# Kernel optimization log

Hardware: AMD Instinct MI355X
Metric: run time of the kernel (lower is better)

Reference implementation:

```python
import jax, jax.numpy as jnp
import numpy as np

EMBED_DIM = 1024
NUM_HEADS = 16
HEAD_DIM = EMBED_DIM // NUM_HEADS
FF_DIM = 4096
SPARSITY_FACTOR = 0.1
SPARSITY_THRESHOLD = 0.5
EPS = 1e-5


def layer_norm(x, w, b):
    mu = jnp.mean(x, axis=-1, keepdims=True)
    var = jnp.mean(jnp.square(x - mu), axis=-1, keepdims=True)
    return (x - mu) * jax.lax.rsqrt(var + EPS) * w + b


def setup_inputs() -> dict:
    key = jax.random.key(0)
    ks = jax.random.split(key, 12)
    B, N, C = 8, 1024, EMBED_DIM
    s = 0.02
    return {
        "x": jax.random.normal(ks[0], (B, N, C), jnp.float32),
        "ln1_w": jnp.ones((C,), jnp.float32),
        "ln1_b": jnp.zeros((C,), jnp.float32),
        "qkv_w": jax.random.normal(ks[1], (3 * C, C), jnp.float32) * s,
        "qkv_b": jnp.zeros((3 * C,), jnp.float32),
        "out_w": jax.random.normal(ks[2], (C, C), jnp.float32) * s,
        "out_b": jnp.zeros((C,), jnp.float32),
        "ln2_w": jnp.ones((C,), jnp.float32),
        "ln2_b": jnp.zeros((C,), jnp.float32),
        "w1": jax.random.normal(ks[3], (FF_DIM, C), jnp.float32) * s,
        "b1": jnp.zeros((FF_DIM,), jnp.float32),
        "w2": jax.random.normal(ks[4], (C, FF_DIM), jnp.float32) * s,
        "b2": jnp.zeros((C,), jnp.float32),
        "mask1": jax.random.uniform(ks[5], (B, N, FF_DIM), jnp.float32),
        "mask2": jax.random.uniform(ks[6], (B, N, C), jnp.float32),
        "layer_idx": 0,
    }


def sparse_attention(x, qkv_w, qkv_b, out_w, out_b):
    B, N, C = x.shape
    qkv = (x @ qkv_w.T + qkv_b).reshape(B, N, 3, NUM_HEADS, HEAD_DIM)
    qkv = jnp.transpose(qkv, (2, 0, 3, 1, 4))  # (3,B,H,N,hd)
    q, k, v = qkv[0], qkv[1], qkv[2]
    scale = HEAD_DIM ** (-0.5)
    scores = jnp.einsum("bhnd,bhmd->bhnm", q, k) * scale  # (B,H,N,N)
    k_sparse = int(SPARSITY_FACTOR * N)
    if 0 < k_sparse < N:
        _, idx = jax.lax.top_k(scores, k_sparse)  # (B,H,N,k)
        bi = jnp.arange(B)[:, None, None, None]
        hi = jnp.arange(NUM_HEADS)[None, :, None, None]
        ni = jnp.arange(N)[None, None, :, None]
        mask = jnp.zeros_like(scores).at[bi, hi, ni, idx].set(1.0)
        scores = scores * mask - 1e9 * (1.0 - mask)
    attn = jax.nn.softmax(scores, axis=-1)
    out = jnp.einsum("bhnm,bhmd->bhnd", attn, v)  # (B,H,N,hd)
    out = jnp.transpose(out, (0, 2, 1, 3)).reshape(B, N, C)
    return out @ out_w.T + out_b


def reference(x, ln1_w, ln1_b, qkv_w, qkv_b, out_w, out_b, ln2_w, ln2_b,
              w1, b1, w2, b2, mask1, mask2, layer_idx):
    # Attention block with residual
    x = x + sparse_attention(layer_norm(x, ln1_w, ln1_b), qkv_w, qkv_b, out_w, out_b)
    # Random-masked FFN block with residual
    m1 = (mask1 > SPARSITY_THRESHOLD).astype(x.dtype)
    m2 = (mask2 > SPARSITY_THRESHOLD).astype(x.dtype)
    h = layer_norm(x, ln2_w, ln2_b)
    h = jax.nn.relu((h @ w1.T + b1) * m1)
    h = ((h @ w2.T + b2) * m2)
    x = x + h
    # Symbolic branch: only runs when (layer_idx+1)%4==0 and never modifies x
    # (original ends in `pass`), so it is an identity on the output.
    return x
```

## Files before the change

kernel.cpp:

```cpp
#include <hip/hip_runtime.h>
#include <cstdint>
#include <cstddef>

typedef unsigned short u16;
typedef __bf16 bf16x8 __attribute__((ext_vector_type(8)));
typedef float f32x4 __attribute__((ext_vector_type(4)));

#define GLOBAL_AS __attribute__((address_space(1)))
#define LDS_AS    __attribute__((address_space(3)))

__device__ __forceinline__ float bf2f(u16 v) {
  return __builtin_bit_cast(float, (uint32_t)v << 16);
}
__device__ __forceinline__ u16 f2bf(float f) {
  uint32_t u = __builtin_bit_cast(uint32_t, f);
  u += 0x7FFFu + ((u >> 16) & 1u);
  return (u16)(u >> 16);
}
__device__ __forceinline__ float extload(const void* p, size_t i, int isf) {
  return isf ? ((const float*)p)[i] : bf2f(((const u16*)p)[i]);
}
__device__ __forceinline__ void gl_lds16(const void* g, void* l) {
  __builtin_amdgcn_global_load_lds((const GLOBAL_AS void*)g, (LDS_AS void*)l, 16, 0, 0);
}

__global__ __launch_bounds__(256) void sniff_k(const u16* __restrict__ x, int* __restrict__ flag) {
  const int t = threadIdx.x;
  int cnt = 0;
#pragma unroll
  for (int j = 0; j < 16; ++j) {
    const u16 w = x[t * 16 + j];
    const int e = (w >> 7) & 0xFF;
    cnt += (e >= 0x90) ? 1 : 0;
  }
#pragma unroll
  for (int o = 32; o; o >>= 1) cnt += __shfl_xor(cnt, o);
  __shared__ int red[4];
  if ((t & 63) == 0) red[t >> 6] = cnt;
  __syncthreads();
  if (t == 0) flag[0] = (red[0] + red[1] + red[2] + red[3] > 16) ? 1 : 0;
}

__global__ __launch_bounds__(256) void cvt_k(const void* __restrict__ in, u16* __restrict__ out,
                                             const int* __restrict__ flagp, int n) {
  const int i = (blockIdx.x * 256 + threadIdx.x) * 4;
  if (i >= n) return;
  if (*flagp) {
    const float4 v = *(const float4*)((const float*)in + i);
    out[i] = f2bf(v.x); out[i + 1] = f2bf(v.y); out[i + 2] = f2bf(v.z); out[i + 3] = f2bf(v.w);
  } else {
    *(ushort4*)(out + i) = *(const ushort4*)((const u16*)in + i);
  }
}

template<bool INTF32>
__global__ __launch_bounds__(256) void ln_k(const void* __restrict__ inp,
                                            const void* __restrict__ w,
                                            const void* __restrict__ b,
                                            u16* __restrict__ out,
                                            const int* __restrict__ flagp)
{
  const int isf = *flagp;
  const int row = blockIdx.x;
  const int t = threadIdx.x;
  float x0, x1, x2, x3;
  if (INTF32 || isf) {
    const float4 vv = ((const float4*)((const float*)inp + (size_t)row * 1024))[t];
    x0 = vv.x; x1 = vv.y; x2 = vv.z; x3 = vv.w;
  } else {
    const ushort4 vv = ((const ushort4*)((const u16*)inp + (size_t)row * 1024))[t];
    x0 = bf2f(vv.x); x1 = bf2f(vv.y); x2 = bf2f(vv.z); x3 = bf2f(vv.w);
  }
  float s = x0 + x1 + x2 + x3;
  float sq = x0 * x0 + x1 * x1 + x2 * x2 + x3 * x3;
#pragma unroll
  for (int o = 32; o; o >>= 1) { s += __shfl_xor(s, o); sq += __shfl_xor(sq, o); }
  __shared__ float red[8];
  const int wv = t >> 6;
  if ((t & 63) == 0) { red[wv] = s; red[wv + 4] = sq; }
  __syncthreads();
  s = red[0] + red[1] + red[2] + red[3];
  sq = red[4] + red[5] + red[6] + red[7];
  const float mu = s * (1.0f / 1024.0f);
  const float var = sq * (1.0f / 1024.0f) - mu * mu;
  const float rstd = rsqrtf(var + 1e-5f);
  const int c0 = t * 4;
  u16* o4 = out + (size_t)row * 1024 + c0;
  o4[0] = f2bf((x0 - mu) * rstd * extload(w, c0 + 0, isf) + extload(b, c0 + 0, isf));
  o4[1] = f2bf((x1 - mu) * rstd * extload(w, c0 + 1, isf) + extload(b, c0 + 1, isf));
  o4[2] = f2bf((x2 - mu) * rstd * extload(w, c0 + 2, isf) + extload(b, c0 + 2, isf));
  o4[3] = f2bf((x3 - mu) * rstd * extload(w, c0 + 3, isf) + extload(b, c0 + 3, isf));
}

template<int EPI>
__global__ __launch_bounds__(256, 2) void gemm_bt(
    const u16* __restrict__ A, const u16* __restrict__ B,
    const void* __restrict__ bias, const void* __restrict__ auxb,
    const float* __restrict__ auxf, void* __restrict__ outp,
    int M, int N, int K, const int* __restrict__ flagp)
{
  __shared__ u16 sA[128 * 32];
  __shared__ u16 sB[128 * 32];
  const int t = threadIdx.x;
  const int lane = t & 63;
  const int wv = t >> 6;
  const int wm = (wv >> 1) << 6;
  const int wn = (wv & 1) << 6;
  const int bm = blockIdx.y << 7;
  const int bn = blockIdx.x << 7;

  f32x4 acc[4][4] = {};

  const int ldr = t >> 2;
  const int lseg = t & 3;
  const int fr = lane & 15;
  const int q = lane >> 4;

  for (int kt = 0; kt < K; kt += 32) {
    __syncthreads();
#pragma unroll
    for (int i = 0; i < 2; ++i) {
      const int r = ldr + (i << 6);
      const int sl = lseg ^ ((r >> 1) & 3);
      gl_lds16(A + (size_t)(bm + r) * K + kt + (sl << 3), &sA[(((i << 8) + t) << 3)]);
      gl_lds16(B + (size_t)(bn + r) * K + kt + (sl << 3), &sB[(((i << 8) + t) << 3)]);
    }
    asm volatile("s_waitcnt vmcnt(0)" ::: "memory");
    __syncthreads();

    bf16x8 af[4], bfv[4];
#pragma unroll
    for (int i = 0; i < 4; ++i) {
      const int rr = wm + (i << 4) + fr;
      af[i] = *(const bf16x8*)&sA[(rr << 5) + ((q ^ ((rr >> 1) & 3)) << 3)];
      const int nn = wn + (i << 4) + fr;
      bfv[i] = *(const bf16x8*)&sB[(nn << 5) + ((q ^ ((nn >> 1) & 3)) << 3)];
    }
#pragma unroll
    for (int mi = 0; mi < 4; ++mi)
#pragma unroll
      for (int ni = 0; ni < 4; ++ni)
        acc[mi][ni] = __builtin_amdgcn_mfma_f32_16x16x32_bf16(af[mi], bfv[ni], acc[mi][ni], 0, 0, 0);
  }

  const int isf = *flagp;
#pragma unroll
  for (int mi = 0; mi < 4; ++mi) {
#pragma unroll
    for (int ni = 0; ni < 4; ++ni) {
#pragma unroll
      for (int r = 0; r < 4; ++r) {
        const int gm = bm + wm + (mi << 4) + (q << 2) + r;
        const int gn = bn + wn + (ni << 4) + fr;
        const size_t idx = (size_t)gm * N + gn;
        float v = acc[mi][ni][r] + extload(bias, gn, isf);
        if (EPI == 0) {
          ((u16*)outp)[idx] = f2bf(v);
        } else if (EPI == 1) {
          ((float*)outp)[idx] = v + extload(auxb, idx, isf);
        } else if (EPI == 2) {
          const float keep = extload(auxb, idx, isf) > 0.5f ? 1.0f : 0.0f;
          ((u16*)outp)[idx] = f2bf(fmaxf(v, 0.0f) * keep);
        } else {
          const float keep = extload(auxb, idx, isf) > 0.5f ? 1.0f : 0.0f;
          const float o = auxf[idx] + v * keep;
          if (isf) ((float*)outp)[idx] = o;
          else     ((u16*)outp)[idx] = f2bf(o);
        }
      }
    }
  }
}

__global__ __launch_bounds__(256) void vtrans_k(const u16* __restrict__ qkv,
                                                u16* __restrict__ vt)
{
  __shared__ u16 tile[64][72];
  const int blk = blockIdx.x;
  const int nt = blk & 15, h = (blk >> 4) & 15, b = blk >> 8;
  const int t = threadIdx.x;
#pragma unroll
  for (int it = 0; it < 2; ++it) {
    const int li = it * 256 + t, r = li >> 3, sg = li & 7;
    const uint4 g = *(const uint4*)(qkv + ((size_t)b * 1024 + nt * 64 + r) * 3072 + 2048 + h * 64 + sg * 8);
    *(uint4*)&tile[r][sg * 8] = g;
  }
  __syncthreads();
#pragma unroll
  for (int it = 0; it < 2; ++it) {
    const int li = it * 256 + t, d = li >> 3, sg = li & 7;
    u16 tmp[8];
#pragma unroll
    for (int j = 0; j < 8; ++j) tmp[j] = tile[sg * 8 + j][d];
    *(uint4*)(vt + (((size_t)(b * 16 + h)) * 64 + d) * 1024 + nt * 64 + sg * 8) = *(const uint4*)tmp;
  }
}

__global__ __launch_bounds__(256, 2) void attn_k(const u16* __restrict__ qkv,
                                                 const u16* __restrict__ vt,
                                                 u16* __restrict__ aout)
{
  __shared__ float s_sc[16 * 1028];

  const int t = threadIdx.x;
  const int lane = t & 63;
  const int wv = t >> 6;
  const int bh = blockIdx.x >> 6;
  const int rb = blockIdx.x & 63;
  const int b = bh >> 4, h = bh & 15;
  const size_t row0 = (size_t)b * 1024;
  const int colQ = h * 64;
  const int fr = lane & 15, q = lane >> 4;

  const u16* qrow = qkv + (row0 + rb * 16 + fr) * 3072 + colQ + q * 8;
  const bf16x8 aq0 = *(const bf16x8*)(qrow);
  const bf16x8 aq1 = *(const bf16x8*)(qrow + 32);

  const u16* kbase = qkv + (row0 + wv * 16 + fr) * 3072 + 1024 + colQ + q * 8;
#pragma unroll
  for (int c = 0; c < 16; ++c) {
    const u16* kp = kbase + (size_t)c * 64 * 3072;
    const bf16x8 bk0 = *(const bf16x8*)(kp);
    const bf16x8 bk1 = *(const bf16x8*)(kp + 32);
    f32x4 sacc = {};
    sacc = __builtin_amdgcn_mfma_f32_16x16x32_bf16(aq0, bk0, sacc, 0, 0, 0);
    sacc = __builtin_amdgcn_mfma_f32_16x16x32_bf16(aq1, bk1, sacc, 0, 0, 0);
#pragma unroll
    for (int r = 0; r < 4; ++r)
      s_sc[(q * 4 + r) * 1028 + c * 64 + wv * 16 + fr] = sacc[r];
  }
  __syncthreads();

  float v[4][16];
  const int r0 = wv * 4;
#pragma unroll
  for (int r = 0; r < 4; ++r)
#pragma unroll
    for (int j = 0; j < 16; ++j)
      v[r][j] = s_sc[(r0 + r) * 1028 + j * 64 + lane];
  __syncthreads();

  float mx[4], mn[4], sm[4], sq[4];
#pragma unroll
  for (int r = 0; r < 4; ++r) {
    float a = v[r][0], n_ = v[r][0], ss = 0.f, qq = 0.f;
#pragma unroll
    for (int j = 0; j < 16; ++j) {
      const float x = v[r][j];
      a = fmaxf(a, x); n_ = fminf(n_, x); ss += x; qq += x * x;
    }
    mx[r] = a; mn[r] = n_; sm[r] = ss; sq[r] = qq;
  }
#pragma unroll
  for (int o = 32; o; o >>= 1)
#pragma unroll
    for (int r = 0; r < 4; ++r) {
      mx[r] = fmaxf(mx[r], __shfl_xor(mx[r], o));
      mn[r] = fminf(mn[r], __shfl_xor(mn[r], o));
      sm[r] += __shfl_xor(sm[r], o);
      sq[r] += __shfl_xor(sq[r], o);
    }

  float lo[4], hi[4], tcur[4], texact[4];
  int nlo[4], nhi[4];
  bool done[4];
#pragma unroll
  for (int r = 0; r < 4; ++r) {
    const float mu = sm[r] * (1.0f / 1024.0f);
    const float var = fmaxf(sq[r] * (1.0f / 1024.0f) - mu * mu, 0.0f);
    const float sd = sqrtf(var + 1e-20f);
    lo[r] = mn[r] - fabsf(mn[r]) * 1e-6f - 1e-12f; nlo[r] = 1024;
    hi[r] = mx[r] + fabsf(mx[r]) * 1e-6f + 1e-12f; nhi[r] = 0;
    const float t0 = mu + 1.2816f * sd;
    const float wdt = hi[r] - lo[r];
    tcur[r] = fminf(fmaxf(t0, lo[r] + 0.02f * wdt), hi[r] - 0.02f * wdt);
    done[r] = false; texact[r] = 0.f;
  }

  for (int it = 0; it < 10; ++it) {
    if (done[0] && done[1] && done[2] && done[3]) break;
    int cc[4];
#pragma unroll
    for (int r = 0; r < 4; ++r) {
      int c_ = 0;
#pragma unroll
      for (int j = 0; j < 16; ++j) c_ += (v[r][j] >= tcur[r]) ? 1 : 0;
      cc[r] = c_;
    }
#pragma unroll
    for (int o = 32; o; o >>= 1)
#pragma unroll
      for (int r = 0; r < 4; ++r) cc[r] += __shfl_xor(cc[r], o);
#pragma unroll
    for (int r = 0; r < 4; ++r) {
      if (!done[r]) {
        if (cc[r] == 102) { done[r] = true; texact[r] = tcur[r]; }
        else if (cc[r] > 102) { lo[r] = tcur[r]; nlo[r] = cc[r]; }
        else { hi[r] = tcur[r]; nhi[r] = cc[r]; }
        float tn;
        if (it & 1) tn = 0.5f * (lo[r] + hi[r]);
        else {
          const float den = (float)(nlo[r] - nhi[r]);
          tn = lo[r] + (hi[r] - lo[r]) * ((float)(nlo[r] - 102) / den);
        }
        const float wdt = hi[r] - lo[r];
        tcur[r] = fminf(fmaxf(tn, lo[r] + 0.02f * wdt), hi[r] - 0.02f * wdt);
      }
    }
  }

  const float CEXP = 0.125f * 1.44269504f;
  const uint64_t ltmask = (1ull << lane) - 1ull;
#pragma unroll
  for (int r = 0; r < 4; ++r) {
    bool kf[16];
    if (done[r]) {
#pragma unroll
      for (int j = 0; j < 16; ++j) kf[j] = (v[r][j] >= texact[r]);
    } else {
#pragma unroll
      for (int j = 0; j < 16; ++j) kf[j] = (v[r][j] >= hi[r]);
      const int need = 102 - nhi[r];
      int taken = 0;
      for (int j = 0; j < 16; ++j) {
        const bool band = (v[r][j] >= lo[r]) && (v[r][j] < hi[r]);
        const uint64_t mk = __ballot(band);
        const int before = (int)__popcll(mk & ltmask);
        if (band && (taken + before) < need) kf[j] = true;
        taken += (int)__popcll(mk);
      }
    }
    float e[16], es = 0.f;
#pragma unroll
    for (int j = 0; j < 16; ++j) {
      e[j] = kf[j] ? exp2f((v[r][j] - mx[r]) * CEXP) : 0.0f;
      es += e[j];
    }
#pragma unroll
    for (int o = 32; o; o >>= 1) es += __shfl_xor(es, o);
    const float inv = 1.0f / es;
    u16* prow = ((u16*)s_sc) + (size_t)(r0 + r) * 1032;
#pragma unroll
    for (int j = 0; j < 16; ++j) prow[j * 64 + lane] = f2bf(e[j] * inv);
  }
  __syncthreads();

  const u16* vtb = vt + (((size_t)(b * 16 + h)) * 64 + wv * 16 + fr) * 1024 + q * 8;
  const u16* pbase = ((const u16*)s_sc) + fr * 1032 + q * 8;
  f32x4 oacc = {};
#pragma unroll
  for (int c = 0; c < 16; ++c) {
    const bf16x8 ap0 = *(const bf16x8*)(pbase + c * 64);
    const bf16x8 ap1 = *(const bf16x8*)(pbase + c * 64 + 32);
    const bf16x8 bv0 = *(const bf16x8*)(vtb + c * 64);
    const bf16x8 bv1 = *(const bf16x8*)(vtb + c * 64 + 32);
    oacc = __builtin_amdgcn_mfma_f32_16x16x32_bf16(ap0, bv0, oacc, 0, 0, 0);
    oacc = __builtin_amdgcn_mfma_f32_16x16x32_bf16(ap1, bv1, oacc, 0, 0, 0);
  }
#pragma unroll
  for (int r = 0; r < 4; ++r)
    aout[(row0 + rb * 16 + q * 4 + r) * 1024 + colQ + wv * 16 + fr] = f2bf(oacc[r]);
}

extern "C" void kernel_launch(void* const* d_in, const int* in_sizes, int n_in,
                              void* d_out, int out_size, void* d_ws, size_t ws_size,
                              hipStream_t stream)
{
  (void)in_sizes; (void)n_in; (void)out_size; (void)ws_size;
  const void* x     = d_in[0];
  const void* ln1w  = d_in[1];
  const void* ln1b  = d_in[2];
  const void* qkvw  = d_in[3];
  const void* qkvb  = d_in[4];
  const void* outw  = d_in[5];
  const void* outb  = d_in[6];
  const void* ln2w  = d_in[7];
  const void* ln2b  = d_in[8];
  const void* w1    = d_in[9];
  const void* b1    = d_in[10];
  const void* w2    = d_in[11];
  const void* b2    = d_in[12];
  const void* mask1 = d_in[13];
  const void* mask2 = d_in[14];

  char* ws = (char*)d_ws;
  const size_t MB = 1ull << 20;
  u16*   xn1    = (u16*)(ws);
  u16*   qkv    = (u16*)(ws + 16 * MB);
  u16*   xn2    = qkv;
  u16*   w1c    = (u16*)(ws + 32 * MB);
  u16*   w2c    = (u16*)(ws + 40 * MB);
  float* x2     = (float*)(ws + 64 * MB);
  u16*   h1     = (u16*)(ws + 96 * MB);
  u16*   wq     = (u16*)(ws + 96 * MB);
  u16*   wo     = (u16*)(ws + 102 * MB);
  u16*   vt     = (u16*)(ws + 104 * MB);
  int*   flagp  = (int*)(ws + 160 * MB);
  u16*   attn_o = xn1;

  sniff_k<<<1, 256, 0, stream>>>((const u16*)x, flagp);
  cvt_k<<<3072, 256, 0, stream>>>(qkvw, wq, flagp, 3072 * 1024);
  cvt_k<<<1024, 256, 0, stream>>>(outw, wo, flagp, 1024 * 1024);

  ln_k<false><<<8192, 256, 0, stream>>>(x, ln1w, ln1b, xn1, flagp);
  gemm_bt<0><<<dim3(24, 64), 256, 0, stream>>>(xn1, wq, qkvb, nullptr, nullptr, qkv, 8192, 3072, 1024, flagp);
  vtrans_k<<<2048, 256, 0, stream>>>(qkv, vt);
  attn_k<<<8192, 256, 0, stream>>>(qkv, vt, attn_o);
  gemm_bt<1><<<dim3(8, 64), 256, 0, stream>>>(attn_o, wo, outb, x, nullptr, x2, 8192, 1024, 1024, flagp);

  cvt_k<<<4096, 256, 0, stream>>>(w1, w1c, flagp, 4096 * 1024);
  cvt_k<<<4096, 256, 0, stream>>>(w2, w2c, flagp, 4096 * 1024);

  ln_k<true><<<8192, 256, 0, stream>>>(x2, ln2w, ln2b, xn2, flagp);
  gemm_bt<2><<<dim3(32, 64), 256, 0, stream>>>(xn2, w1c, b1, mask1, nullptr, h1, 8192, 4096, 1024, flagp);
  gemm_bt<3><<<dim3(8, 64), 256, 0, stream>>>(h1, w2c, b2, mask2, x2, d_out, 8192, 1024, 4096, flagp);
}
```

Before: 1.226 ms.

## Keep attention scores in registers via transposed MFMA, shrink LDS for occupancy

The score tile is now computed as K·Q^T so each lane holds 64 scores of one query row in registers, which removes the fp32 LDS staging of the full 16x1024 score block. Row statistics, threshold counts and softmax sums are reduced within a wave by shuffles and across waves through small LDS arrays with barriers. The smaller LDS footprint allows launch bounds of 4 blocks per CU, and block IDs are swizzled to group blocks by batch-head. In exchange each threshold iteration now needs a block-wide barrier, and the tie-band selection order changes.

```diff
diff --git a/kernel.cpp b/kernel.cpp
--- a/kernel.cpp
+++ b/kernel.cpp
@@ -196,157 +196,184 @@
   }
 }
 
-__global__ __launch_bounds__(256, 2) void attn_k(const u16* __restrict__ qkv,
+__global__ __launch_bounds__(256, 4) void attn_k(const u16* __restrict__ qkv,
                                                  const u16* __restrict__ vt,
                                                  u16* __restrict__ aout)
 {
-  __shared__ float s_sc[16 * 1028];
+  __shared__ u16 sP[16 * 1032];
+  __shared__ float4 red4[4][16];
+  __shared__ uint cntb[2][4][16];
+  __shared__ uint fcnt[4][16];
+  __shared__ float esred[4][16];
 
   const int t = threadIdx.x;
   const int lane = t & 63;
   const int wv = t >> 6;
-  const int bh = blockIdx.x >> 6;
-  const int rb = blockIdx.x & 63;
+  const int bid = blockIdx.x;
+  const int sw = ((bid & 7) << 10) | (bid >> 3);
+  const int bh = sw >> 6;
+  const int rb = sw & 63;
   const int b = bh >> 4, h = bh & 15;
   const size_t row0 = (size_t)b * 1024;
   const int colQ = h * 64;
   const int fr = lane & 15, q = lane >> 4;
 
   const u16* qrow = qkv + (row0 + rb * 16 + fr) * 3072 + colQ + q * 8;
-  const bf16x8 aq0 = *(const bf16x8*)(qrow);
-  const bf16x8 aq1 = *(const bf16x8*)(qrow + 32);
-
-  const u16* kbase = qkv + (row0 + wv * 16 + fr) * 3072 + 1024 + colQ + q * 8;
-#pragma unroll
-  for (int c = 0; c < 16; ++c) {
-    const u16* kp = kbase + (size_t)c * 64 * 3072;
-    const bf16x8 bk0 = *(const bf16x8*)(kp);
-    const bf16x8 bk1 = *(const bf16x8*)(kp + 32);
+  const bf16x8 bq0 = *(const bf16x8*)(qrow);
+  const bf16x8 bq1 = *(const bf16x8*)(qrow + 32);
+
+  float v2[16][4];
+  const u16* kbase = qkv + (row0 + wv * 256 + fr) * 3072 + 1024 + colQ + q * 8;
+#pragma unroll
+  for (int tt = 0; tt < 16; ++tt) {
+    const u16* kp = kbase + (size_t)tt * 16 * 3072;
+    const bf16x8 ak0 = *(const bf16x8*)(kp);
+    const bf16x8 ak1 = *(const bf16x8*)(kp + 32);
     f32x4 sacc = {};
-    sacc = __builtin_amdgcn_mfma_f32_16x16x32_bf16(aq0, bk0, sacc, 0, 0, 0);
-    sacc = __builtin_amdgcn_mfma_f32_16x16x32_bf16(aq1, bk1, sacc, 0, 0, 0);
-#pragma unroll
-    for (int r = 0; r < 4; ++r)
-      s_sc[(q * 4 + r) * 1028 + c * 64 + wv * 16 + fr] = sacc[r];
-  }
-  __syncthreads();
-
-  float v[4][16];
-  const int r0 = wv * 4;
-#pragma unroll
-  for (int r = 0; r < 4; ++r)
-#pragma unroll
-    for (int j = 0; j < 16; ++j)
-      v[r][j] = s_sc[(r0 + r) * 1028 + j * 64 + lane];
-  __syncthreads();
-
-  float mx[4], mn[4], sm[4], sq[4];
-#pragma unroll
-  for (int r = 0; r < 4; ++r) {
-    float a = v[r][0], n_ = v[r][0], ss = 0.f, qq = 0.f;
-#pragma unroll
-    for (int j = 0; j < 16; ++j) {
-      const float x = v[r][j];
-      a = fmaxf(a, x); n_ = fminf(n_, x); ss += x; qq += x * x;
-    }
-    mx[r] = a; mn[r] = n_; sm[r] = ss; sq[r] = qq;
-  }
-#pragma unroll
-  for (int o = 32; o; o >>= 1)
+    sacc = __builtin_amdgcn_mfma_f32_16x16x32_bf16(ak0, bq0, sacc, 0, 0, 0);
+    sacc = __builtin_amdgcn_mfma_f32_16x16x32_bf16(ak1, bq1, sacc, 0, 0, 0);
+#pragma unroll
+    for (int r = 0; r < 4; ++r) v2[tt][r] = sacc[r];
+  }
+
+  float mx = v2[0][0], mn = v2[0][0], sm = 0.f, sq = 0.f;
+#pragma unroll
+  for (int tt = 0; tt < 16; ++tt)
 #pragma unroll
     for (int r = 0; r < 4; ++r) {
-      mx[r] = fmaxf(mx[r], __shfl_xor(mx[r], o));
-      mn[r] = fminf(mn[r], __shfl_xor(mn[r], o));
-      sm[r] += __shfl_xor(sm[r], o);
-      sq[r] += __shfl_xor(sq[r], o);
-    }
-
-  float lo[4], hi[4], tcur[4], texact[4];
-  int nlo[4], nhi[4];
-  bool done[4];
-#pragma unroll
-  for (int r = 0; r < 4; ++r) {
-    const float mu = sm[r] * (1.0f / 1024.0f);
-    const float var = fmaxf(sq[r] * (1.0f / 1024.0f) - mu * mu, 0.0f);
+      const float x = v2[tt][r];
+      mx = fmaxf(mx, x); mn = fminf(mn, x); sm += x; sq += x * x;
+    }
+  mx = fmaxf(mx, __shfl_xor(mx, 16)); mx = fmaxf(mx, __shfl_xor(mx, 32));
+  mn = fminf(mn, __shfl_xor(mn, 16)); mn = fminf(mn, __shfl_xor(mn, 32));
+  sm += __shfl_xor(sm, 16); sm += __shfl_xor(sm, 32);
+  sq += __shfl_xor(sq, 16); sq += __shfl_xor(sq, 32);
+  if (lane < 16) red4[wv][fr] = make_float4(mx, mn, sm, sq);
+  __syncthreads();
+  {
+    const float4 a0 = red4[0][fr], a1 = red4[1][fr], a2 = red4[2][fr], a3 = red4[3][fr];
+    mx = fmaxf(fmaxf(a0.x, a1.x), fmaxf(a2.x, a3.x));
+    mn = fminf(fminf(a0.y, a1.y), fminf(a2.y, a3.y));
+    sm = a0.z + a1.z + a2.z + a3.z;
+    sq = a0.w + a1.w + a2.w + a3.w;
+  }
+
+  float lo, hi, tcur, texact = 0.f;
+  int nlo = 1024, nhi = 0;
+  bool done = false;
+  {
+    const float mu = sm * (1.0f / 1024.0f);
+    const float var = fmaxf(sq * (1.0f / 1024.0f) - mu * mu, 0.0f);
     const float sd = sqrtf(var + 1e-20f);
-    lo[r] = mn[r] - fabsf(mn[r]) * 1e-6f - 1e-12f; nlo[r] = 1024;
-    hi[r] = mx[r] + fabsf(mx[r]) * 1e-6f + 1e-12f; nhi[r] = 0;
+    lo = mn - fabsf(mn) * 1e-6f - 1e-12f;
+    hi = mx + fabsf(mx) * 1e-6f + 1e-12f;
     const float t0 = mu + 1.2816f * sd;
-    const float wdt = hi[r] - lo[r];
-    tcur[r] = fminf(fmaxf(t0, lo[r] + 0.02f * wdt), hi[r] - 0.02f * wdt);
-    done[r] = false; texact[r] = 0.f;
+    const float wdt = hi - lo;
+    tcur = fminf(fmaxf(t0, lo + 0.02f * wdt), hi - 0.02f * wdt);
   }
 
   for (int it = 0; it < 10; ++it) {
-    if (done[0] && done[1] && done[2] && done[3]) break;
-    int cc[4];
+    if (__ballot(!done) == 0ull) break;
+    int c_ = 0;
+#pragma unroll
+    for (int tt = 0; tt < 16; ++tt)
+#pragma unroll
+      for (int r = 0; r < 4; ++r) c_ += (v2[tt][r] >= tcur) ? 1 : 0;
+    c_ += __shfl_xor(c_, 16); c_ += __shfl_xor(c_, 32);
+    if (lane < 16) cntb[it & 1][wv][fr] = (uint)c_;
+    __syncthreads();
+    const int cc = (int)(cntb[it & 1][0][fr] + cntb[it & 1][1][fr] +
+                         cntb[it & 1][2][fr] + cntb[it & 1][3][fr]);
+    if (!done) {
+      if (cc == 102) { done = true; texact = tcur; }
+      else if (cc > 102) { lo = tcur; nlo = cc; }
+      else { hi = tcur; nhi = cc; }
+      float tn;
+      if (it & 1) tn = 0.5f * (lo + hi);
+      else {
+        const float den = (float)(nlo - nhi);
+        tn = lo + (hi - lo) * ((float)(nlo - 102) / den);
+      }
+      const float wdt = hi - lo;
+      tcur = fminf(fmaxf(tn, lo + 0.02f * wdt), hi - 0.02f * wdt);
+    }
+  }
+
+  uint64_t kmask = 0ull;
+  const uint64_t anymask = __ballot(!done);
+  if (anymask == 0ull) {
+#pragma unroll
+    for (int tt = 0; tt < 16; ++tt)
+#pragma unroll
+      for (int r = 0; r < 4; ++r)
+        if (v2[tt][r] >= texact) kmask |= 1ull << (tt * 4 + r);
+  } else {
+    const float thr = done ? texact : hi;
+    int bc = 0;
+#pragma unroll
+    for (int tt = 0; tt < 16; ++tt)
+#pragma unroll
+      for (int r = 0; r < 4; ++r) {
+        const float x = v2[tt][r];
+        if (x >= thr) kmask |= 1ull << (tt * 4 + r);
+        bc += (!done && x >= lo && x < hi) ? 1 : 0;
+      }
+    int bw = bc + __shfl_xor(bc, 16);
+    bw += __shfl_xor(bw, 32);
+    if (lane < 16) fcnt[wv][fr] = (uint)bw;
+    __syncthreads();
+    if (!done) {
+      int pre = 0;
+#pragma unroll
+      for (int w = 0; w < 4; ++w) if (w < wv) pre += (int)fcnt[w][fr];
+#pragma unroll
+      for (int qq = 0; qq < 3; ++qq) {
+        const int ov = __shfl(bc, fr + 16 * qq);
+        if (qq < q) pre += ov;
+      }
+      const int need = 102 - nhi;
+#pragma unroll
+      for (int tt = 0; tt < 16; ++tt)
+#pragma unroll
+        for (int r = 0; r < 4; ++r) {
+          const float x = v2[tt][r];
+          if (x >= lo && x < hi) {
+            if (pre < need) kmask |= 1ull << (tt * 4 + r);
+            ++pre;
+          }
+        }
+    }
+  }
+
+  const float CEXP = 0.125f * 1.44269504f;
+  float es = 0.f;
+#pragma unroll
+  for (int tt = 0; tt < 16; ++tt)
 #pragma unroll
     for (int r = 0; r < 4; ++r) {
-      int c_ = 0;
-#pragma unroll
-      for (int j = 0; j < 16; ++j) c_ += (v[r][j] >= tcur[r]) ? 1 : 0;
-      cc[r] = c_;
-    }
-#pragma unroll
-    for (int o = 32; o; o >>= 1)
-#pragma unroll
-      for (int r = 0; r < 4; ++r) cc[r] += __shfl_xor(cc[r], o);
-#pragma unroll
-    for (int r = 0; r < 4; ++r) {
-      if (!done[r]) {
-        if (cc[r] == 102) { done[r] = true; texact[r] = tcur[r]; }
-        else if (cc[r] > 102) { lo[r] = tcur[r]; nlo[r] = cc[r]; }
-        else { hi[r] = tcur[r]; nhi[r] = cc[r]; }
-        float tn;
-        if (it & 1) tn = 0.5f * (lo[r] + hi[r]);
-        else {
-          const float den = (float)(nlo[r] - nhi[r]);
-          tn = lo[r] + (hi[r] - lo[r]) * ((float)(nlo[r] - 102) / den);
-        }
-        const float wdt = hi[r] - lo[r];
-        tcur[r] = fminf(fmaxf(tn, lo[r] + 0.02f * wdt), hi[r] - 0.02f * wdt);
-      }
-    }
-  }
-
-  const float CEXP = 0.125f * 1.44269504f;
-  const uint64_t ltmask = (1ull << lane) - 1ull;
-#pragma unroll
-  for (int r = 0; r < 4; ++r) {
-    bool kf[16];
-    if (done[r]) {
-#pragma unroll
-      for (int j = 0; j < 16; ++j) kf[j] = (v[r][j] >= texact[r]);
-    } else {
-#pragma unroll
-      for (int j = 0; j < 16; ++j) kf[j] = (v[r][j] >= hi[r]);
-      const int need = 102 - nhi[r];
-      int taken = 0;
-      for (int j = 0; j < 16; ++j) {
-        const bool band = (v[r][j] >= lo[r]) && (v[r][j] < hi[r]);
-        const uint64_t mk = __ballot(band);
-        const int before = (int)__popcll(mk & ltmask);
-        if (band && (taken + before) < need) kf[j] = true;
-        taken += (int)__popcll(mk);
-      }
-    }
-    float e[16], es = 0.f;
-#pragma unroll
-    for (int j = 0; j < 16; ++j) {
-      e[j] = kf[j] ? exp2f((v[r][j] - mx[r]) * CEXP) : 0.0f;
-      es += e[j];
-    }
-#pragma unroll
-    for (int o = 32; o; o >>= 1) es += __shfl_xor(es, o);
-    const float inv = 1.0f / es;
-    u16* prow = ((u16*)s_sc) + (size_t)(r0 + r) * 1032;
-#pragma unroll
-    for (int j = 0; j < 16; ++j) prow[j * 64 + lane] = f2bf(e[j] * inv);
+      const float e = ((kmask >> (tt * 4 + r)) & 1ull) ? exp2f((v2[tt][r] - mx) * CEXP) : 0.0f;
+      v2[tt][r] = e;
+      es += e;
+    }
+  es += __shfl_xor(es, 16); es += __shfl_xor(es, 32);
+  if (lane < 16) esred[wv][fr] = es;
+  __syncthreads();
+  const float inv = 1.0f / (esred[0][fr] + esred[1][fr] + esred[2][fr] + esred[3][fr]);
+
+  u16* prow = sP + (size_t)fr * 1032 + wv * 256;
+#pragma unroll
+  for (int tt = 0; tt < 16; ++tt) {
+#pragma unroll
+    for (int rp = 0; rp < 2; ++rp) {
+      const u16 p0 = f2bf(v2[tt][2 * rp] * inv);
+      const u16 p1 = f2bf(v2[tt][2 * rp + 1] * inv);
+      *(uint*)(prow + tt * 16 + q * 4 + 2 * rp) = (uint)p0 | ((uint)p1 << 16);
+    }
   }
   __syncthreads();
 
   const u16* vtb = vt + (((size_t)(b * 16 + h)) * 64 + wv * 16 + fr) * 1024 + q * 8;
-  const u16* pbase = ((const u16*)s_sc) + fr * 1032 + q * 8;
+  const u16* pbase = sP + fr * 1032 + q * 8;
   f32x4 oacc = {};
 #pragma unroll
   for (int c = 0; c < 16; ++c) {
```

Result: faster. 1.030 ms (-16.0%).
